# Optimization experiments

Hardware: AMD Instinct MI355X
Metric: run time of the kernel (lower is better)

The kernel has to match this reference:

```python
import jax, jax.numpy as jnp
import numpy as np

N_NODES = 50000
EPS_NORM = 1e-12
EPS_ENT = 1e-8

def _l2norm(x):
    # torch.nn.functional.normalize: x / clamp(||x||, min=1e-12)
    n = jnp.sqrt(jnp.sum(x * x, axis=-1, keepdims=True))
    return x / jnp.maximum(n, EPS_NORM)

def _layer(hidden, src, dst, edge_type, multi_emb, proto_emb):
    # hidden: [N,H]; multi_emb: [R,P,H]; proto_emb: [P,H]
    inp_j = hidden[src]                          # [E,H] gather
    rel_basis = multi_emb[edge_type]             # [E,P,H] gather
    sims = jnp.einsum('eh,ph->ep', _l2norm(inp_j), _l2norm(proto_emb))  # cosine sim [E,P]
    proto_proba = jax.nn.softmax(sims, axis=1)   # [E,P]
    msg = jnp.einsum('ep,eph->eh', proto_proba, rel_basis)              # [E,H]
    ent = -jnp.sum(proto_proba * jnp.log(proto_proba + EPS_ENT), axis=1)  # [E]
    logits = -ent
    # scatter_softmax over destination index
    seg_max = jax.ops.segment_max(logits, dst, num_segments=N_NODES)
    ex = jnp.exp(logits - seg_max[dst])
    denom = jax.ops.segment_sum(ex, dst, num_segments=N_NODES)
    attn = ex / denom[dst]                       # [E]
    out = jax.ops.segment_sum(attn[:, None] * msg, dst, num_segments=N_NODES)  # [N,H]
    return out

def setup_inputs() -> dict:
    key = jax.random.key(0)
    ks = jax.random.split(key, 6)
    E = 800000
    H, R, P, L = 128, 18, 18, 3  # num_layers=4 -> 3 NBFCluttr layers
    edge_index = jax.random.randint(ks[0], (2, E), 0, N_NODES, dtype=jnp.int64) if jax.config.read('jax_enable_x64') else jax.random.randint(ks[0], (2, E), 0, N_NODES, dtype=jnp.int32)
    edge_type = jax.random.randint(ks[1], (E,), 0, R, dtype=edge_index.dtype)
    tail_indices = jax.random.randint(ks[2], (1024,), 0, N_NODES, dtype=edge_index.dtype)
    multi_embeddings = jax.random.uniform(ks[3], (L, R, P, H), dtype=jnp.float32)
    proto_embeddings = jax.random.uniform(ks[4], (L, P, H), dtype=jnp.float32)
    source_embedding = jax.random.uniform(ks[5], (H,), dtype=jnp.float32)
    return {"edge_index": edge_index, "edge_type": edge_type, "tail_indices": tail_indices,
            "multi_embeddings": multi_embeddings, "proto_embeddings": proto_embeddings,
            "source_embedding": source_embedding}

def reference(edge_index, edge_type, tail_indices, multi_embeddings, proto_embeddings, source_embedding):
    src, dst = edge_index[0], edge_index[1]
    H = source_embedding.shape[0]
    # boundary condition: source node gets source_embedding, rest zero
    hidden = jnp.zeros((N_NODES, H), dtype=source_embedding.dtype).at[0].set(source_embedding)
    L = multi_embeddings.shape[0]
    for l in range(L):  # small fixed loop over structurally distinct layers
        hidden = _layer(hidden, src, dst, edge_type, multi_embeddings[l], proto_embeddings[l])
    # apply_classifier, eval_mode=True, use_mlp_classifier=False -> cosine sims to last layer prototypes
    out_emb = hidden[tail_indices]               # [B,H]
    sims = jnp.einsum('nh,ph->np', _l2norm(out_emb), _l2norm(proto_embeddings[-1]))
    return sims  # gumbel_softmax_sample with eval_mode=True returns logits unchanged
```

## Files before the change

### kernel.cpp

```cpp
#include <hip/hip_runtime.h>
#include <hip/hip_bf16.h>


#define N_NODES 50000
#define H 128
#define P 18
#define RP 324
#define KPAD 352
#define K0PAD 64
#define ELLW 64
#define NPART 8
#define NODES_PER_PART 6250

typedef _Float16 half8 __attribute__((ext_vector_type(8)));
typedef _Float16 half4 __attribute__((ext_vector_type(4)));
typedef float floatx4 __attribute__((ext_vector_type(4)));

__global__ __launch_bounds__(256) void ell_kernel(const int* __restrict__ src,
                                                  const int* __restrict__ dst,
                                                  const int* __restrict__ etype,
                                                  unsigned* __restrict__ cur,
                                                  unsigned* __restrict__ ep, int E) {
  int part = blockIdx.x & (NPART - 1);
  int i = (blockIdx.x >> 3) * 256 + threadIdx.x;
  if (i >= E) return;
  int d = dst[i];
  int lo = part * NODES_PER_PART;
  if (d < lo || d >= lo + NODES_PER_PART) return;
  unsigned pos = atomicAdd(&cur[d], 1u);
  if (pos < ELLW)
    ep[(size_t)d * ELLW + pos] = (unsigned)src[i] | ((unsigned)etype[i] << 20);
}

__global__ __launch_bounds__(64) void protoq0_kernel(const float* __restrict__ proto,
                                                     const float* __restrict__ semb,
                                                     float* __restrict__ pN,
                                                     float* __restrict__ q0r) {
  int row = blockIdx.x, l = threadIdx.x;
  if (row < 54) {
    float a = proto[row * H + l], b = proto[row * H + 64 + l];
    float ss = a * a + b * b;
    for (int m = 32; m > 0; m >>= 1) ss += __shfl_xor(ss, m, 64);
    float inv = 1.f / fmaxf(sqrtf(ss), 1e-12f);
    pN[row * H + l] = a * inv;
    pN[row * H + 64 + l] = b * inv;
    return;
  }
  float s0 = semb[l], s1 = semb[l + 64];
  float ss = s0 * s0 + s1 * s1;
  float dot[P];
#pragma unroll
  for (int p = 0; p < P; p++) {
    float a = proto[p * H + l], b = proto[p * H + 64 + l];
    float rn = a * a + b * b;
    for (int m = 32; m > 0; m >>= 1) rn += __shfl_xor(rn, m, 64);
    float rinv = 1.f / fmaxf(sqrtf(rn), 1e-12f);
    dot[p] = (s0 * a + s1 * b) * rinv;
  }
  for (int m = 1; m <= 32; m <<= 1) {
    ss += __shfl_xor(ss, m, 64);
#pragma unroll
    for (int p = 0; p < P; p++) dot[p] += __shfl_xor(dot[p], m, 64);
  }
  float inv = 1.f / fmaxf(sqrtf(ss), 1e-12f);
  float sum = 0.f;
#pragma unroll
  for (int p = 0; p < P; p++) {
    dot[p] = __expf(dot[p] * inv - 1.f);
    sum += dot[p];
  }
  float isum = 1.f / sum, ent = 0.f;
#pragma unroll
  for (int p = 0; p < P; p++) {
    dot[p] *= isum;
    ent -= dot[p] * __logf(dot[p] + 1e-8f);
  }
  float w = __expf(-ent);
  if (l < P) q0r[l] = w * dot[l];
}

__global__ __launch_bounds__(256) void bprep_kernel(const float* __restrict__ multi,
                                                    const float* __restrict__ q0r,
                                                    _Float16* __restrict__ Btg,
                                                    _Float16* __restrict__ Btl0,
                                                    unsigned* __restrict__ cur) {
  int idx = blockIdx.x * 256 + threadIdx.x;
  if (idx < N_NODES) cur[idx] = 0u;
  if (idx < 2 * H * KPAD) {
    int l = idx / (H * KPAD), rem = idx - l * (H * KPAD);
    int h = rem / KPAD, k = rem - h * KPAD;
    const float* B = multi + (size_t)(l + 1) * RP * H;
    Btg[idx] = (k < RP) ? (_Float16)B[k * H + h] : (_Float16)0.f;
    return;
  }
  int idx2 = idx - 2 * H * KPAD;
  if (idx2 >= H * K0PAD) return;
  int h = idx2 >> 6, k = idx2 & 63;
  float pr = 1.f / 18.f, ent = 0.f;
#pragma unroll
  for (int p = 0; p < P; p++) ent -= pr * __logf(pr + 1e-8f);
  float qc = __expf(-ent) * pr;
  float v = 0.f;
  if (k < P) {
#pragma unroll
    for (int p = 0; p < P; p++) v += qc * multi[(k * P + p) * H + h];
  } else if (k < 2 * P) {
    int r = k - P;
#pragma unroll
    for (int p = 0; p < P; p++) v += (q0r[p] - qc) * multi[(r * P + p) * H + h];
  }
  Btl0[h * K0PAD + k] = (_Float16)v;
}

__global__ __launch_bounds__(256) void hist_kernel(const unsigned* __restrict__ ep,
                                                   const unsigned* __restrict__ cur,
                                                   _Float16* __restrict__ M, int n) {
  int wave = threadIdx.x >> 6, lane = threadIdx.x & 63;
  int nd = blockIdx.x * 4 + wave;
  if (nd >= n) return;
  int cnt = (int)cur[nd];
  if (cnt > ELLW) cnt = ELLW;
  bool a = lane < cnt;
  unsigned pk = a ? ep[(size_t)nd * ELLW + lane] : 0xFFFFFFFFu;
  int r = (int)(pk >> 20);
  unsigned long long zm = __ballot(a && (pk & 0xFFFFFu) == 0u);
  float creg = 0.f, creg0 = 0.f;
#pragma unroll
  for (int rr = 0; rr < P; rr++) {
    unsigned long long m = __ballot(a && (r == rr));
    if (lane == rr) {
      creg = (float)__popcll(m);
      creg0 = (float)__popcll(m & zm);
    }
  }
  int slx = (lane >= P && lane < 2 * P) ? lane - P : 0;
  float v0 = __shfl(creg0, slx, 64);
  float val = (lane < P) ? creg : ((lane < 2 * P) ? v0 : 0.f);
  M[(size_t)nd * K0PAD + lane] = (_Float16)val;
}

__global__ __launch_bounds__(256) void scatter_kernel(const unsigned* __restrict__ ep,
                                                      const unsigned* __restrict__ cur,
                                                      const _Float16* __restrict__ q,
                                                      const int* __restrict__ tl,
                                                      _Float16* __restrict__ M, int n) {
  __shared__ float sl[4][3 * RP];
  int wave = threadIdx.x >> 6, lane = threadIdx.x & 63;
  int t = blockIdx.x * 4 + wave;
  float* s0 = sl[wave];
  for (int i = lane; i < 3 * RP; i += 64) s0[i] = 0.f;
  int cnt = 0;
  size_t b = 0;
  if (t < n) {
    int nd = tl ? tl[t] : t;
    b = (size_t)nd * ELLW;
    cnt = (int)cur[nd];
    if (cnt > ELLW) cnt = ELLW;
  }
  unsigned eload = 0xFFFFFFFFu;
  if (t < n && lane < cnt) eload = ep[b + lane];
  int sub = lane / 18;
  int j = lane - sub * 18;
  bool act = (sub < 3) && (t < n);
  float* ms = s0 + (sub < 3 ? sub : 0) * RP;
  for (int base = 0; base < cnt; base += 24) {
    unsigned pk[8];
    float qv[8];
    bool av[8];
#pragma unroll
    for (int u = 0; u < 8; u++) {
      int e = base + sub + 3 * u;
      av[u] = act && (e < cnt);
      pk[u] = __shfl(eload, e & 63, 64);
      qv[u] = 0.f;
      if (av[u]) qv[u] = (float)q[(size_t)(pk[u] & 0xFFFFFu) * P + j];
    }
#pragma unroll
    for (int u = 0; u < 8; u++)
      if (av[u]) ms[(pk[u] >> 20) * P + j] += qv[u];
  }
  if (t < n) {
    for (int k = lane; k < RP; k += 64)
      M[(size_t)t * KPAD + k] = (_Float16)(s0[k] + s0[RP + k] + s0[2 * RP + k]);
    for (int k = RP + lane; k < KPAD; k += 64) M[(size_t)t * KPAD + k] = (_Float16)0.f;
  }
}

template <int MODE>
__global__ __launch_bounds__(256) void gemm_kernel(const _Float16* __restrict__ M,
                                                   const _Float16* __restrict__ Bt,
                                                   const float* __restrict__ pN,
                                                   void* __restrict__ out_ptr, int n,
                                                   int kpad) {
  __shared__ _Float16 smem_h[64 * 132];
  _Float16* As = smem_h;
  _Float16* Bs = smem_h + 2048;
  int tid = threadIdx.x;
  int wave = tid >> 6, lane = tid & 63;
  int m15 = lane & 15, quad = lane >> 4;
  int n0 = blockIdx.x * 64;
  floatx4 acc[4][2] = {};

  __shared__ float pns[4 * P * 36];
  for (int i = tid; i < 4 * P * 32; i += 256) {
    int s = i / (P * 32), r = i - s * (P * 32);
    int p = r >> 5, kk = r & 31;
    pns[s * (P * 36) + p * 36 + kk] = pN[p * H + s * 32 + kk];
  }

  for (int kt = 0; kt < (kpad >> 5); kt++) {
    int k0 = kt * 32;
    __syncthreads();
    {
      int row = tid >> 2, kc = (tid & 3) * 8;
      int gr = n0 + row;
      half8 v = {};
      if (gr < n) v = *(const half8*)(M + (size_t)gr * kpad + k0 + kc);
      *(half8*)(As + row * 32 + kc) = v;
    }
    {
      int col = tid >> 1, kc = (tid & 1) * 16;
      const _Float16* srcp = Bt + (size_t)col * kpad + k0 + kc;
      *(half8*)(Bs + col * 32 + kc) = *(const half8*)srcp;
      *(half8*)(Bs + col * 32 + kc + 8) = *(const half8*)(srcp + 8);
    }
    __syncthreads();
    half8 bfrag0 = *(const half8*)(Bs + (wave * 32 + m15) * 32 + quad * 8);
    half8 bfrag1 = *(const half8*)(Bs + (wave * 32 + 16 + m15) * 32 + quad * 8);
#pragma unroll
    for (int mt = 0; mt < 4; mt++) {
      half8 afrag = *(const half8*)(As + (mt * 16 + m15) * 32 + quad * 8);
      acc[mt][0] = __builtin_amdgcn_mfma_f32_16x16x32_f16(afrag, bfrag0, acc[mt][0], 0, 0, 0);
      acc[mt][1] = __builtin_amdgcn_mfma_f32_16x16x32_f16(afrag, bfrag1, acc[mt][1], 0, 0, 0);
    }
  }
  __syncthreads();
#pragma unroll
  for (int mt = 0; mt < 4; mt++)
#pragma unroll
    for (int c = 0; c < 2; c++)
#pragma unroll
      for (int reg = 0; reg < 4; reg++)
        smem_h[(mt * 16 + quad * 4 + reg) * 132 + wave * 32 + c * 16 + m15] =
            (_Float16)acc[mt][c][reg];
  __syncthreads();
  int node = tid >> 2, sub = tid & 3;
  int gnode = n0 + node;
  const _Float16* trow = smem_h + node * 132 + sub * 32;
  const float* ps = pns + sub * (P * 36);
  float ss = 0.f;
  float dot[P];
#pragma unroll
  for (int p = 0; p < P; p++) dot[p] = 0.f;
#pragma unroll
  for (int k4 = 0; k4 < 8; k4++) {
    half4 yh = *(const half4*)(trow + k4 * 4);
    float y0 = (float)yh.x, y1 = (float)yh.y, y2 = (float)yh.z, y3 = (float)yh.w;
    ss += y0 * y0 + y1 * y1 + y2 * y2 + y3 * y3;
#pragma unroll
    for (int p = 0; p < P; p++) {
      float4 bb = *(const float4*)(ps + p * 36 + k4 * 4);
      dot[p] += y0 * bb.x + y1 * bb.y + y2 * bb.z + y3 * bb.w;
    }
  }
  for (int m = 1; m <= 2; m <<= 1) {
    ss += __shfl_xor(ss, m, 64);
#pragma unroll
    for (int p = 0; p < P; p++) dot[p] += __shfl_xor(dot[p], m, 64);
  }
  if (gnode < n) {
    float inv = 1.f / fmaxf(sqrtf(ss), 1e-12f);
    if (MODE == 1) {
      float* outp = (float*)out_ptr;
      for (int p = sub; p < P; p += 4) outp[(size_t)gnode * P + p] = dot[p] * inv;
    } else {
      float sum = 0.f;
#pragma unroll
      for (int p = 0; p < P; p++) {
        dot[p] = __expf(dot[p] * inv - 1.f);
        sum += dot[p];
      }
      float isum = 1.f / sum, ent = 0.f;
#pragma unroll
      for (int p = 0; p < P; p++) {
        dot[p] *= isum;
        ent -= dot[p] * __logf(dot[p] + 1e-8f);
      }
      float w = __expf(-ent);
      _Float16* qp = (_Float16*)out_ptr;
      for (int p = sub; p < P; p += 4) qp[(size_t)gnode * P + p] = (_Float16)(w * dot[p]);
    }
  }
}

extern "C" void kernel_launch(void* const* d_in, const int* in_sizes, int n_in,
                              void* d_out, int out_size, void* d_ws, size_t ws_size,
                              hipStream_t stream) {
  const int* eidx = (const int*)d_in[0];
  int E = in_sizes[0] / 2;
  const int* src = eidx;
  const int* dst = eidx + E;
  const int* etype = (const int*)d_in[1];
  const int* tails = (const int*)d_in[2];
  int T = in_sizes[2];
  const float* multi = (const float*)d_in[3];
  const float* proto = (const float*)d_in[4];
  const float* semb = (const float*)d_in[5];
  float* out = (float*)d_out;

  char* w = (char*)d_ws;
  auto alloc = [&](size_t bytes) {
    char* p = w;
    w += (bytes + 255) & ~(size_t)255;
    return p;
  };
  _Float16* q = (_Float16*)alloc((size_t)N_NODES * P * 2);
  float* q0r = (float*)alloc((size_t)P * 4);
  float* pNs = (float*)alloc((size_t)3 * P * H * 4);
  _Float16* Mg = (_Float16*)alloc((size_t)N_NODES * KPAD * 2);
  _Float16* Btg = (_Float16*)alloc((size_t)2 * H * KPAD * 2);
  _Float16* Btl0 = (_Float16*)alloc((size_t)H * K0PAD * 2);
  unsigned* cur = (unsigned*)alloc((size_t)N_NODES * 4);
  unsigned* ep = (unsigned*)alloc((size_t)N_NODES * ELLW * 4);

  int eb = (E + 255) / 256;

  protoq0_kernel<<<55, 64, 0, stream>>>(proto, semb, pNs, q0r);
  bprep_kernel<<<(2 * H * KPAD + H * K0PAD + 255) / 256, 256, 0, stream>>>(multi, q0r, Btg,
                                                                           Btl0, cur);

  ell_kernel<<<eb * NPART, 256, 0, stream>>>(src, dst, etype, cur, ep, E);

  hist_kernel<<<(N_NODES + 3) / 4, 256, 0, stream>>>(ep, cur, Mg, N_NODES);
  gemm_kernel<0><<<(N_NODES + 63) / 64, 256, 0, stream>>>(Mg, Btl0, pNs + (size_t)1 * P * H, q,
                                                          N_NODES, K0PAD);

  scatter_kernel<<<(N_NODES + 3) / 4, 256, 0, stream>>>(ep, cur, q, nullptr, Mg, N_NODES);
  gemm_kernel<0><<<(N_NODES + 63) / 64, 256, 0, stream>>>(Mg, Btg, pNs + (size_t)2 * P * H, q,
                                                          N_NODES, KPAD);

  scatter_kernel<<<(T + 3) / 4, 256, 0, stream>>>(ep, cur, q, tails, Mg, T);
  gemm_kernel<1><<<(T + 63) / 64, 256, 0, stream>>>(Mg, Btg + (size_t)H * KPAD,
                                                    pNs + (size_t)2 * P * H, out, T, KPAD);
}
```

Baseline: 238.5 us.

## Merge prototype and B-matrix prep kernels; store prototypes as fp16 in LDS

Folds the prototype-normalization/q0 kernel and the B-transpose prep kernel into one launch. Blocks are partitioned by index, and the q0 weights are computed redundantly per Btl0 block into shared memory. It also stores the normalized prototypes in LDS as fp16 inside the GEMM epilogue, halving LDS footprint and read traffic for the cosine-similarity dot products. This saves a launch and possibly raises occupancy, at the cost of some precision in the similarity scores.

Measured after the change: 239.9 us. About the same (+0.6%).

```diff
diff --git a/kernel.cpp b/kernel.cpp
--- a/kernel.cpp
+++ b/kernel.cpp
@@ -32,68 +32,74 @@
     ep[(size_t)d * ELLW + pos] = (unsigned)src[i] | ((unsigned)etype[i] << 20);
 }
 
-__global__ __launch_bounds__(64) void protoq0_kernel(const float* __restrict__ proto,
-                                                     const float* __restrict__ semb,
-                                                     float* __restrict__ pN,
-                                                     float* __restrict__ q0r) {
-  int row = blockIdx.x, l = threadIdx.x;
-  if (row < 54) {
-    float a = proto[row * H + l], b = proto[row * H + 64 + l];
-    float ss = a * a + b * b;
-    for (int m = 32; m > 0; m >>= 1) ss += __shfl_xor(ss, m, 64);
-    float inv = 1.f / fmaxf(sqrtf(ss), 1e-12f);
-    pN[row * H + l] = a * inv;
-    pN[row * H + 64 + l] = b * inv;
+__global__ __launch_bounds__(256) void prep_kernel(const float* __restrict__ proto,
+                                                   const float* __restrict__ semb,
+                                                   const float* __restrict__ multi,
+                                                   float* __restrict__ pN,
+                                                   _Float16* __restrict__ Btg,
+                                                   _Float16* __restrict__ Btl0,
+                                                   unsigned* __restrict__ cur) {
+  int bid = blockIdx.x, tid = threadIdx.x;
+  int gi = bid * 256 + tid;
+  if (gi < N_NODES) cur[gi] = 0u;
+
+  if (bid < 54) {
+    if (tid < 64) {
+      int row = bid, l = tid;
+      float a = proto[row * H + l], b = proto[row * H + 64 + l];
+      float ss = a * a + b * b;
+      for (int m = 32; m > 0; m >>= 1) ss += __shfl_xor(ss, m, 64);
+      float inv = 1.f / fmaxf(sqrtf(ss), 1e-12f);
+      pN[row * H + l] = a * inv;
+      pN[row * H + 64 + l] = b * inv;
+    }
     return;
   }
-  float s0 = semb[l], s1 = semb[l + 64];
-  float ss = s0 * s0 + s1 * s1;
-  float dot[P];
-#pragma unroll
-  for (int p = 0; p < P; p++) {
-    float a = proto[p * H + l], b = proto[p * H + 64 + l];
-    float rn = a * a + b * b;
-    for (int m = 32; m > 0; m >>= 1) rn += __shfl_xor(rn, m, 64);
-    float rinv = 1.f / fmaxf(sqrtf(rn), 1e-12f);
-    dot[p] = (s0 * a + s1 * b) * rinv;
-  }
-  for (int m = 1; m <= 32; m <<= 1) {
-    ss += __shfl_xor(ss, m, 64);
-#pragma unroll
-    for (int p = 0; p < P; p++) dot[p] += __shfl_xor(dot[p], m, 64);
-  }
-  float inv = 1.f / fmaxf(sqrtf(ss), 1e-12f);
-  float sum = 0.f;
-#pragma unroll
-  for (int p = 0; p < P; p++) {
-    dot[p] = __expf(dot[p] * inv - 1.f);
-    sum += dot[p];
-  }
-  float isum = 1.f / sum, ent = 0.f;
-#pragma unroll
-  for (int p = 0; p < P; p++) {
-    dot[p] *= isum;
-    ent -= dot[p] * __logf(dot[p] + 1e-8f);
-  }
-  float w = __expf(-ent);
-  if (l < P) q0r[l] = w * dot[l];
-}
-
-__global__ __launch_bounds__(256) void bprep_kernel(const float* __restrict__ multi,
-                                                    const float* __restrict__ q0r,
-                                                    _Float16* __restrict__ Btg,
-                                                    _Float16* __restrict__ Btl0,
-                                                    unsigned* __restrict__ cur) {
-  int idx = blockIdx.x * 256 + threadIdx.x;
-  if (idx < N_NODES) cur[idx] = 0u;
-  if (idx < 2 * H * KPAD) {
+  if (bid < 406) {
+    int idx = (bid - 54) * 256 + tid;
     int l = idx / (H * KPAD), rem = idx - l * (H * KPAD);
     int h = rem / KPAD, k = rem - h * KPAD;
     const float* B = multi + (size_t)(l + 1) * RP * H;
     Btg[idx] = (k < RP) ? (_Float16)B[k * H + h] : (_Float16)0.f;
     return;
   }
-  int idx2 = idx - 2 * H * KPAD;
+  __shared__ float qs[P];
+  if (tid < 64) {
+    int l = tid;
+    float s0 = semb[l], s1 = semb[l + 64];
+    float ss = s0 * s0 + s1 * s1;
+    float dot[P];
+#pragma unroll
+    for (int p = 0; p < P; p++) {
+      float a = proto[p * H + l], b = proto[p * H + 64 + l];
+      float rn = a * a + b * b;
+      for (int m = 32; m > 0; m >>= 1) rn += __shfl_xor(rn, m, 64);
+      float rinv = 1.f / fmaxf(sqrtf(rn), 1e-12f);
+      dot[p] = (s0 * a + s1 * b) * rinv;
+    }
+    for (int m = 1; m <= 32; m <<= 1) {
+      ss += __shfl_xor(ss, m, 64);
+#pragma unroll
+      for (int p = 0; p < P; p++) dot[p] += __shfl_xor(dot[p], m, 64);
+    }
+    float inv = 1.f / fmaxf(sqrtf(ss), 1e-12f);
+    float sum = 0.f;
+#pragma unroll
+    for (int p = 0; p < P; p++) {
+      dot[p] = __expf(dot[p] * inv - 1.f);
+      sum += dot[p];
+    }
+    float isum = 1.f / sum, ent = 0.f;
+#pragma unroll
+    for (int p = 0; p < P; p++) {
+      dot[p] *= isum;
+      ent -= dot[p] * __logf(dot[p] + 1e-8f);
+    }
+    float w = __expf(-ent);
+    if (l < P) qs[l] = w * dot[l];
+  }
+  __syncthreads();
+  int idx2 = (bid - 406) * 256 + tid;
   if (idx2 >= H * K0PAD) return;
   int h = idx2 >> 6, k = idx2 & 63;
   float pr = 1.f / 18.f, ent = 0.f;
@@ -107,7 +113,7 @@
   } else if (k < 2 * P) {
     int r = k - P;
 #pragma unroll
-    for (int p = 0; p < P; p++) v += (q0r[p] - qc) * multi[(r * P + p) * H + h];
+    for (int p = 0; p < P; p++) v += (qs[p] - qc) * multi[(r * P + p) * H + h];
   }
   Btl0[h * K0PAD + k] = (_Float16)v;
 }
@@ -201,11 +207,11 @@
   int n0 = blockIdx.x * 64;
   floatx4 acc[4][2] = {};
 
-  __shared__ float pns[4 * P * 36];
+  __shared__ _Float16 pns[4 * P * 36];
   for (int i = tid; i < 4 * P * 32; i += 256) {
     int s = i / (P * 32), r = i - s * (P * 32);
     int p = r >> 5, kk = r & 31;
-    pns[s * (P * 36) + p * 36 + kk] = pN[p * H + s * 32 + kk];
+    pns[s * (P * 36) + p * 36 + kk] = (_Float16)pN[p * H + s * 32 + kk];
   }
 
   for (int kt = 0; kt < (kpad >> 5); kt++) {
@@ -247,7 +253,7 @@
   int node = tid >> 2, sub = tid & 3;
   int gnode = n0 + node;
   const _Float16* trow = smem_h + node * 132 + sub * 32;
-  const float* ps = pns + sub * (P * 36);
+  const _Float16* ps = pns + sub * (P * 36);
   float ss = 0.f;
   float dot[P];
 #pragma unroll
@@ -259,8 +265,8 @@
     ss += y0 * y0 + y1 * y1 + y2 * y2 + y3 * y3;
 #pragma unroll
     for (int p = 0; p < P; p++) {
-      float4 bb = *(const float4*)(ps + p * 36 + k4 * 4);
-      dot[p] += y0 * bb.x + y1 * bb.y + y2 * bb.z + y3 * bb.w;
+      half4 bh = *(const half4*)(ps + p * 36 + k4 * 4);
+      dot[p] += y0 * (float)bh.x + y1 * (float)bh.y + y2 * (float)bh.z + y3 * (float)bh.w;
     }
   }
   for (int m = 1; m <= 2; m <<= 1) {
@@ -315,7 +321,6 @@
     return p;
   };
   _Float16* q = (_Float16*)alloc((size_t)N_NODES * P * 2);
-  float* q0r = (float*)alloc((size_t)P * 4);
   float* pNs = (float*)alloc((size_t)3 * P * H * 4);
   _Float16* Mg = (_Float16*)alloc((size_t)N_NODES * KPAD * 2);
   _Float16* Btg = (_Float16*)alloc((size_t)2 * H * KPAD * 2);
@@ -325,9 +330,7 @@
 
   int eb = (E + 255) / 256;
 
-  protoq0_kernel<<<55, 64, 0, stream>>>(proto, semb, pNs, q0r);
-  bprep_kernel<<<(2 * H * KPAD + H * K0PAD + 255) / 256, 256, 0, stream>>>(multi, q0r, Btg,
-                                                                           Btl0, cur);
+  prep_kernel<<<438, 256, 0, stream>>>(proto, semb, multi, pNs, Btg, Btl0, cur);
 
   ell_kernel<<<eb * NPART, 256, 0, stream>>>(src, dst, etype, cur, ep, E);
 
```
